# Optimization experiments

Measured on AMD Instinct MI355X. Metric: run time of the kernel, lower is better.

## Reference

```python
import jax, jax.numpy as jnp
import numpy as np

B, T, V, F, NH = 2, 1, 4, 128, 9
EMB_ZOOM = 5
N = 12 * 4 ** EMB_ZOOM        # 12288 grid cells at emb_zoom
NUP = 4 * N                   # 49152 cells at zoom emb_zoom+1
NVARS = 8


def setup_inputs() -> dict:
    key = jax.random.key(0)
    ks = jax.random.split(key, 8)
    embeddings = jax.random.normal(ks[0], (NVARS, N, F), dtype=jnp.float32)
    x5 = jax.random.normal(ks[1], (B, T, V, N, F), dtype=jnp.float32)
    x6 = jax.random.normal(ks[2], (B, T, V, NUP, F), dtype=jnp.float32)
    W5 = jax.random.normal(ks[3], (F, 2 * F), dtype=jnp.float32) / np.sqrt(F)
    b5 = jnp.zeros((2 * F,), dtype=jnp.float32)
    W6 = jax.random.normal(ks[4], (NH * F, 8 * F), dtype=jnp.float32) / np.sqrt(NH * F)
    b6 = jnp.zeros((8 * F,), dtype=jnp.float32)
    var_idx = jax.random.randint(ks[5], (B, T, V), 0, NVARS)
    adjc = jax.random.randint(ks[6], (N, NH), 0, N)
    adjc = adjc.at[:, 0].set(jnp.arange(N))  # column 0 is the self index
    return {"embeddings": embeddings, "x5": x5, "x6": x6,
            "W5": W5, "b5": b5, "W6": W6, "b6": b6,
            "var_idx": var_idx, "adjc": adjc}


def reference(embeddings, x5, x6, W5, b5, W6, b6, var_idx, adjc):
    # per-variable embedding selection: (B,T,V,N,F)
    embs = embeddings[var_idx]

    # --- zoom == emb_zoom: gather self index, Linear(F -> 2F), FiLM ---
    e5 = jnp.take(embs, adjc[:, 0], axis=-2)          # (B,T,V,N,F)
    h5 = e5 @ W5 + b5                                  # (B,T,V,N,2F)
    scale5, shift5 = jnp.split(h5, 2, axis=-1)
    y5 = x5 * scale5 + shift5

    # --- zoom == emb_zoom+1: gather full neighborhood, Linear(9F -> 4*2F), FiLM ---
    e6 = jnp.take(embs, adjc.reshape(-1), axis=-2)     # (B,T,V,N*NH,F)
    e6 = e6.reshape(B, T, V, N, NH * F)
    h6 = (e6 @ W6 + b6).reshape(B, T, V, NUP, 2 * F)   # 4 children per coarse cell
    scale6, shift6 = jnp.split(h6, 2, axis=-1)
    y6 = x6 * scale6 + shift6

    return (y5, y6)
```

## Files before the change

### kernel.cpp

```cpp
#include <hip/hip_runtime.h>
#include <stdint.h>

#define F_     128
#define N_     12288
#define NH_    9
#define NSLOT_ 8
#define NVARS_ 8
#define NUP_   (4*N_)
#define K6_    (NH_*F_)
#define NC6_   1024

typedef __attribute__((ext_vector_type(8))) short bf16x8;
typedef __attribute__((ext_vector_type(4))) float f32x4;

typedef const __attribute__((address_space(1))) unsigned char* gp1_t;
typedef __attribute__((address_space(3))) unsigned char* lp3_t;

__device__ __forceinline__ void load16(const void* g, void* l) {
  __builtin_amdgcn_global_load_lds((gp1_t)g, (lp3_t)l, 16, 0, 0);
}

__device__ __forceinline__ unsigned short f2bf(float f) {
  union { float f; unsigned int u; } x; x.f = f;
  unsigned int u = x.u;
  unsigned int r = u + 0x7FFFu + ((u >> 16) & 1u);
  return (unsigned short)(r >> 16);
}

__global__ void k_conv_emb(const float4* __restrict__ src, ushort4* __restrict__ dst, int n4) {
  int i = blockIdx.x * blockDim.x + threadIdx.x;
  if (i >= n4) return;
  float4 v = src[i];
  ushort4 o;
  o.x = f2bf(v.x); o.y = f2bf(v.y); o.z = f2bf(v.z); o.w = f2bf(v.w);
  dst[i] = o;
}

__global__ void k_transpose_bf(const float* __restrict__ src, unsigned short* __restrict__ dst,
                               int rows, int cols) {
  int i = blockIdx.x * blockDim.x + threadIdx.x;
  if (i >= rows * cols) return;
  int j = i / rows, k = i % rows;
  dst[i] = f2bf(src[k * cols + j]);
}

__global__ __launch_bounds__(256) void k_h5(
    const unsigned short* __restrict__ embB,
    const unsigned short* __restrict__ W5T,
    const float* __restrict__ b5,
    const float* __restrict__ x5,
    const int* __restrict__ var_idx,
    const int* __restrict__ adjc,
    float* __restrict__ y5)
{
  __shared__ __align__(1024) unsigned char smem[8192 + 32768 + 64*4];
  unsigned char* Asm = smem;
  unsigned char* Bsm = smem + 8192;
  int* ald = (int*)(smem + 8192 + 32768);

  const int tid = threadIdx.x;
  const int l = tid & 63, w = tid >> 6;
  const int wr = w >> 1, wc = w & 1;
  const int li8 = l >> 3, pc = l & 7, l15 = l & 15, l16 = l >> 4;

  const int nt = blockIdx.x, slot = blockIdx.y;
  const int n0 = nt * 64;
  const int var = var_idx[slot];

  if (tid < 64) ald[tid] = adjc[(n0 + tid) * NH_];
  __syncthreads();

  const f32x4 fz = {0.f, 0.f, 0.f, 0.f};
  f32x4 accS[2][4], accH[2][4];
#pragma unroll
  for (int mf = 0; mf < 2; ++mf)
#pragma unroll
    for (int nf = 0; nf < 4; ++nf) { accS[mf][nf] = fz; accH[mf][nf] = fz; }

  const size_t embVarOff = (size_t)var * ((size_t)N_ * F_);

  for (int step = 0; step < 2; ++step) {
    const int k0 = step << 6;
#pragma unroll
    for (int q2 = 0; q2 < 2; ++q2) {
      const int q = w * 2 + q2;
      const int r = q * 8 + li8;
      const int lc = pc ^ (r & 7);
      const unsigned short* g = embB + embVarOff + (size_t)ald[r] * F_ + k0 + lc * 8;
      load16(g, Asm + q * 1024);
    }
#pragma unroll
    for (int q2 = 0; q2 < 8; ++q2) {
      const int q = w * 8 + q2;
      const int j = q * 8 + li8;
      const int lc = pc ^ (j & 7);
      const unsigned short* g = W5T + (size_t)j * F_ + k0 + lc * 8;
      load16(g, Bsm + q * 1024);
    }
    __syncthreads();

#pragma unroll
    for (int kf = 0; kf < 2; ++kf) {
      const int kc = kf * 4 + l16;
      bf16x8 a[2], bs[4], bh[4];
#pragma unroll
      for (int mf = 0; mf < 2; ++mf) {
        const int r = wr * 32 + mf * 16 + l15;
        a[mf] = *(const bf16x8*)(Asm + r * 128 + ((kc ^ (r & 7)) << 4));
      }
#pragma unroll
      for (int nf = 0; nf < 4; ++nf) {
        const int js = wc * 64 + nf * 16 + l15;
        bs[nf] = *(const bf16x8*)(Bsm + js * 128 + ((kc ^ (js & 7)) << 4));
        const int jh = js + 128;
        bh[nf] = *(const bf16x8*)(Bsm + jh * 128 + ((kc ^ (jh & 7)) << 4));
      }
#pragma unroll
      for (int mf = 0; mf < 2; ++mf)
#pragma unroll
        for (int nf = 0; nf < 4; ++nf) {
          accS[mf][nf] = __builtin_amdgcn_mfma_f32_16x16x32_bf16(a[mf], bs[nf], accS[mf][nf], 0, 0, 0);
          accH[mf][nf] = __builtin_amdgcn_mfma_f32_16x16x32_bf16(a[mf], bh[nf], accH[mf][nf], 0, 0, 0);
        }
    }
    __syncthreads();
  }

#pragma unroll
  for (int mf = 0; mf < 2; ++mf)
#pragma unroll
    for (int nf = 0; nf < 4; ++nf) {
      const int f = wc * 64 + nf * 16 + l15;
      const float sb = b5[f];
      const float hb = b5[128 + f];
#pragma unroll
      for (int reg = 0; reg < 4; ++reg) {
        const int r = wr * 32 + mf * 16 + l16 * 4 + reg;
        const int n = n0 + r;
        const size_t idx = ((size_t)slot * N_ + n) * F_ + f;
        y5[idx] = x5[idx] * (accS[mf][nf][reg] + sb) + (accH[mf][nf][reg] + hb);
      }
    }
}

__global__ __launch_bounds__(512) void k_h6(
    const unsigned short* __restrict__ embB,
    const unsigned short* __restrict__ W6T,
    const float* __restrict__ b6,
    const float* __restrict__ x6,
    const int* __restrict__ var_idx,
    const int* __restrict__ adjc,
    float* __restrict__ y6)
{
  __shared__ __align__(1024) unsigned char smem[16384 + 32768 + K6_*4];
  unsigned char* Asm = smem;
  unsigned char* Bsm = smem + 16384;
  int* ald = (int*)(smem + 16384 + 32768);

  const int tid = threadIdx.x;
  const int l = tid & 63, w = tid >> 6;
  const int wr = w >> 2, wc = w & 3;
  const int li8 = l >> 3, pc = l & 7, l15 = l & 15, l16 = l >> 4;

  const int nt = blockIdx.x;
  const int ct = blockIdx.y;
  const int slot = blockIdx.z;
  const int n0 = nt * 128;
  const int col0 = ct * 256;
  const int var = var_idx[slot];

  for (int t = tid; t < 128 * NH_; t += 512) ald[t] = adjc[n0 * NH_ + t];
  __syncthreads();

  const f32x4 fz = {0.f, 0.f, 0.f, 0.f};
  f32x4 accS[4][2], accH[4][2];
#pragma unroll
  for (int mf = 0; mf < 4; ++mf)
#pragma unroll
    for (int nf = 0; nf < 2; ++nf) { accS[mf][nf] = fz; accH[mf][nf] = fz; }

  const size_t embVarOff = (size_t)var * ((size_t)N_ * F_);

  for (int step = 0; step < K6_ / 64; ++step) {
    const int h = step >> 1;
    const int kk0 = (step & 1) << 6;
    const int k0 = step << 6;

#pragma unroll
    for (int q2 = 0; q2 < 2; ++q2) {
      const int q = w * 2 + q2;
      const int r = q * 8 + li8;
      const int lc = pc ^ (r & 7);
      const int m = ald[r * NH_ + h];
      const unsigned short* g = embB + embVarOff + (size_t)m * F_ + kk0 + lc * 8;
      load16(g, Asm + q * 1024);
    }
#pragma unroll
    for (int q2 = 0; q2 < 4; ++q2) {
      const int q = w * 4 + q2;
      const int j = q * 8 + li8;
      const int lc = pc ^ (j & 7);
      const unsigned short* g = W6T + (size_t)(col0 + j) * K6_ + k0 + lc * 8;
      load16(g, Bsm + q * 1024);
    }
    __syncthreads();

#pragma unroll
    for (int kf = 0; kf < 2; ++kf) {
      const int kc = kf * 4 + l16;
      bf16x8 a[4], bs[2], bh[2];
#pragma unroll
      for (int mf = 0; mf < 4; ++mf) {
        const int r = wr * 64 + mf * 16 + l15;
        a[mf] = *(const bf16x8*)(Asm + r * 128 + ((kc ^ (r & 7)) << 4));
      }
#pragma unroll
      for (int nf = 0; nf < 2; ++nf) {
        const int js = wc * 32 + nf * 16 + l15;
        bs[nf] = *(const bf16x8*)(Bsm + js * 128 + ((kc ^ (js & 7)) << 4));
        const int jh = js + 128;
        bh[nf] = *(const bf16x8*)(Bsm + jh * 128 + ((kc ^ (jh & 7)) << 4));
      }
#pragma unroll
      for (int mf = 0; mf < 4; ++mf)
#pragma unroll
        for (int nf = 0; nf < 2; ++nf) {
          accS[mf][nf] = __builtin_amdgcn_mfma_f32_16x16x32_bf16(a[mf], bs[nf], accS[mf][nf], 0, 0, 0);
          accH[mf][nf] = __builtin_amdgcn_mfma_f32_16x16x32_bf16(a[mf], bh[nf], accH[mf][nf], 0, 0, 0);
        }
    }
    __syncthreads();
  }

#pragma unroll
  for (int mf = 0; mf < 4; ++mf)
#pragma unroll
    for (int nf = 0; nf < 2; ++nf) {
      const int f = wc * 32 + nf * 16 + l15;
      const float sb = b6[col0 + f];
      const float hb = b6[col0 + 128 + f];
#pragma unroll
      for (int reg = 0; reg < 4; ++reg) {
        const int r = wr * 64 + mf * 16 + l16 * 4 + reg;
        const int nup = 4 * (n0 + r) + ct;
        const size_t idx = ((size_t)slot * NUP_ + nup) * F_ + f;
        y6[idx] = x6[idx] * (accS[mf][nf][reg] + sb) + (accH[mf][nf][reg] + hb);
      }
    }
}

extern "C" void kernel_launch(void* const* d_in, const int* in_sizes, int n_in,
                              void* d_out, int out_size, void* d_ws, size_t ws_size,
                              hipStream_t stream) {
  (void)in_sizes; (void)n_in; (void)out_size; (void)ws_size;
  const float* emb = (const float*)d_in[0];
  const float* x5  = (const float*)d_in[1];
  const float* x6  = (const float*)d_in[2];
  const float* W5  = (const float*)d_in[3];
  const float* b5  = (const float*)d_in[4];
  const float* W6  = (const float*)d_in[5];
  const float* b6  = (const float*)d_in[6];
  const int* var_idx = (const int*)d_in[7];
  const int* adjc    = (const int*)d_in[8];

  float* y5 = (float*)d_out;
  float* y6 = y5 + (size_t)NSLOT_ * N_ * F_;

  unsigned short* embB = (unsigned short*)d_ws;
  unsigned short* W5T  = embB + (size_t)NVARS_ * N_ * F_;
  unsigned short* W6T  = W5T + 256 * 128;

  const int embN4 = NVARS_ * N_ * F_ / 4;
  k_conv_emb<<<(embN4 + 255) / 256, 256, 0, stream>>>((const float4*)emb, (ushort4*)embB, embN4);
  k_transpose_bf<<<(128 * 256 + 255) / 256, 256, 0, stream>>>(W5, W5T, 128, 256);
  k_transpose_bf<<<(1152 * 1024 + 255) / 256, 256, 0, stream>>>(W6, W6T, 1152, 1024);

  k_h5<<<dim3(N_ / 64, NSLOT_), 256, 0, stream>>>(embB, W5T, b5, x5, var_idx, adjc, y5);
  k_h6<<<dim3(N_ / 128, 4, NSLOT_), 512, 0, stream>>>(embB, W6T, b6, x6, var_idx, adjc, y6);
}
```

Measured before the change: 309.7 us.

## Double-buffer h6 GEMM with 256-row tiles, staged loads, and block swizzle

Rewrites the k_h6 main loop as a double-buffered, 8-wave pipeline. Each block now handles 256 rows instead of 128, and the gather loads for the next K-step are issued in quarter-stages between MFMA phases, using explicit vmcnt/lgkmcnt waits, barriers and setprio. Block IDs are remapped so consecutive blocks spread across XCDs, and launch bounds request 2 blocks per CU. The aim is to hide global-to-LDS latency and reuse each B tile over more rows. In exchange the kernel uses about 137KB of LDS and twice the accumulator registers, which may limit occupancy.

Result: slower. 336.7 us (+8.7%).

```diff
diff --git a/kernel.cpp b/kernel.cpp
--- a/kernel.cpp
+++ b/kernel.cpp
@@ -8,7 +8,7 @@
 #define NVARS_ 8
 #define NUP_   (4*N_)
 #define K6_    (NH_*F_)
-#define NC6_   1024
+#define NSTEP6 (K6_/64)
 
 typedef __attribute__((ext_vector_type(8))) short bf16x8;
 typedef __attribute__((ext_vector_type(4))) float f32x4;
@@ -143,7 +143,7 @@
     }
 }
 
-__global__ __launch_bounds__(512) void k_h6(
+__global__ __launch_bounds__(512, 2) void k_h6(
     const unsigned short* __restrict__ embB,
     const unsigned short* __restrict__ W6T,
     const float* __restrict__ b6,
@@ -152,101 +152,171 @@
     const int* __restrict__ adjc,
     float* __restrict__ y6)
 {
-  __shared__ __align__(1024) unsigned char smem[16384 + 32768 + K6_*4];
-  unsigned char* Asm = smem;
-  unsigned char* Bsm = smem + 16384;
-  int* ald = (int*)(smem + 16384 + 32768);
+  __shared__ __align__(1024) unsigned char smem[65536 + 65536 + 256*NH_*4];
+  unsigned char* Asm0 = smem;
+  unsigned char* Bsm0 = smem + 65536;
+  int* ald = (int*)(smem + 131072);
 
   const int tid = threadIdx.x;
   const int l = tid & 63, w = tid >> 6;
   const int wr = w >> 2, wc = w & 3;
   const int li8 = l >> 3, pc = l & 7, l15 = l & 15, l16 = l >> 4;
 
-  const int nt = blockIdx.x;
-  const int ct = blockIdx.y;
-  const int slot = blockIdx.z;
-  const int n0 = nt * 128;
+  int bid = blockIdx.x + 48 * (blockIdx.y + 4 * blockIdx.z);
+  bid = (bid & 7) * (1536 / 8) + (bid >> 3);
+  const int nt = bid % 48;
+  const int ct = (bid / 48) & 3;
+  const int slot = bid / 192;
+
+  const int n0 = nt * 256;
   const int col0 = ct * 256;
   const int var = var_idx[slot];
-
-  for (int t = tid; t < 128 * NH_; t += 512) ald[t] = adjc[n0 * NH_ + t];
+  const size_t embOff = (size_t)var * ((size_t)N_ * F_);
+
+  for (int t2 = tid; t2 < 256 * NH_; t2 += 512) ald[t2] = adjc[n0 * NH_ + t2];
   __syncthreads();
 
+#define STAGE_A(s, hh, bb) do {                                                   \
+    const int h_ = (s) >> 1; const int kk_ = ((s) & 1) << 6;                      \
+    _Pragma("unroll")                                                             \
+    for (int q2_ = 0; q2_ < 2; ++q2_) {                                           \
+      const int q_ = w * 2 + q2_;                                                 \
+      const int rl_ = (hh) * 128 + q_ * 8 + li8;                                  \
+      const int lc_ = pc ^ (rl_ & 7);                                             \
+      const unsigned short* g_ = embB + embOff + (size_t)ald[rl_ * NH_ + h_] * F_ \
+                                 + kk_ + lc_ * 8;                                 \
+      load16(g_, Asm0 + (bb) * 32768 + (hh) * 16384 + q_ * 1024);                 \
+    } } while (0)
+
+#define STAGE_B(s, hh, bb) do {                                                   \
+    const int k_ = (s) << 6;                                                      \
+    _Pragma("unroll")                                                             \
+    for (int q2_ = 0; q2_ < 2; ++q2_) {                                           \
+      const int q_ = w * 2 + q2_;                                                 \
+      const int jl_ = (hh) * 128 + q_ * 8 + li8;                                  \
+      const int lc_ = pc ^ (jl_ & 7);                                             \
+      const unsigned short* g_ = W6T + (size_t)(col0 + jl_) * K6_ + k_ + lc_ * 8; \
+      load16(g_, Bsm0 + (bb) * 32768 + (hh) * 16384 + q_ * 1024);                 \
+    } } while (0)
+
+#define LDA(dst, mh) do {                                                         \
+    _Pragma("unroll")                                                             \
+    for (int mq_ = 0; mq_ < 4; ++mq_)                                             \
+    _Pragma("unroll")                                                             \
+    for (int kf_ = 0; kf_ < 2; ++kf_) {                                           \
+      const int r_ = (mh) * 128 + wr * 64 + mq_ * 16 + l15;                       \
+      const int kc_ = kf_ * 4 + l16;                                              \
+      dst[mq_][kf_] = *(const bf16x8*)(Ab + r_ * 128 + ((kc_ ^ (r_ & 7)) << 4));  \
+    } } while (0)
+
+#define LDB(dst, jofs) do {                                                       \
+    _Pragma("unroll")                                                             \
+    for (int nf_ = 0; nf_ < 2; ++nf_)                                             \
+    _Pragma("unroll")                                                             \
+    for (int kf_ = 0; kf_ < 2; ++kf_) {                                           \
+      const int j_ = (jofs) + wc * 32 + nf_ * 16 + l15;                           \
+      const int kc_ = kf_ * 4 + l16;                                              \
+      dst[nf_][kf_] = *(const bf16x8*)(Bb + j_ * 128 + ((kc_ ^ (j_ & 7)) << 4));  \
+    } } while (0)
+
+#define MM(acc, mh, af, bfr) do {                                                 \
+    _Pragma("unroll")                                                             \
+    for (int mq_ = 0; mq_ < 4; ++mq_)                                             \
+    _Pragma("unroll")                                                             \
+    for (int nf_ = 0; nf_ < 2; ++nf_)                                             \
+    _Pragma("unroll")                                                             \
+    for (int kf_ = 0; kf_ < 2; ++kf_)                                             \
+      acc[(mh)*4+mq_][nf_] = __builtin_amdgcn_mfma_f32_16x16x32_bf16(             \
+          af[mq_][kf_], bfr[nf_][kf_], acc[(mh)*4+mq_][nf_], 0, 0, 0);            \
+    } while (0)
+
+#define VMCNT4 asm volatile("s_waitcnt vmcnt(4)" ::: "memory")
+#define LGK0   do { asm volatile("s_waitcnt lgkmcnt(0)" ::: "memory"); \
+                    __builtin_amdgcn_sched_barrier(0); } while (0)
+#define BAR    __builtin_amdgcn_s_barrier()
+#define PRIO1  __builtin_amdgcn_s_setprio(1)
+#define PRIO0  __builtin_amdgcn_s_setprio(0)
+
   const f32x4 fz = {0.f, 0.f, 0.f, 0.f};
-  f32x4 accS[4][2], accH[4][2];
-#pragma unroll
-  for (int mf = 0; mf < 4; ++mf)
+  f32x4 accS[8][2], accH[8][2];
+#pragma unroll
+  for (int mf = 0; mf < 8; ++mf)
 #pragma unroll
     for (int nf = 0; nf < 2; ++nf) { accS[mf][nf] = fz; accH[mf][nf] = fz; }
 
-  const size_t embVarOff = (size_t)var * ((size_t)N_ * F_);
-
-  for (int step = 0; step < K6_ / 64; ++step) {
-    const int h = step >> 1;
-    const int kk0 = (step & 1) << 6;
-    const int k0 = step << 6;
-
-#pragma unroll
-    for (int q2 = 0; q2 < 2; ++q2) {
-      const int q = w * 2 + q2;
-      const int r = q * 8 + li8;
-      const int lc = pc ^ (r & 7);
-      const int m = ald[r * NH_ + h];
-      const unsigned short* g = embB + embVarOff + (size_t)m * F_ + kk0 + lc * 8;
-      load16(g, Asm + q * 1024);
-    }
-#pragma unroll
-    for (int q2 = 0; q2 < 4; ++q2) {
-      const int q = w * 4 + q2;
-      const int j = q * 8 + li8;
-      const int lc = pc ^ (j & 7);
-      const unsigned short* g = W6T + (size_t)(col0 + j) * K6_ + k0 + lc * 8;
-      load16(g, Bsm + q * 1024);
-    }
-    __syncthreads();
-
-#pragma unroll
-    for (int kf = 0; kf < 2; ++kf) {
-      const int kc = kf * 4 + l16;
-      bf16x8 a[4], bs[2], bh[2];
-#pragma unroll
-      for (int mf = 0; mf < 4; ++mf) {
-        const int r = wr * 64 + mf * 16 + l15;
-        a[mf] = *(const bf16x8*)(Asm + r * 128 + ((kc ^ (r & 7)) << 4));
+  STAGE_A(0, 0, 0);
+  STAGE_B(0, 0, 0);
+  STAGE_B(0, 1, 0);
+  STAGE_A(0, 1, 0);
+  VMCNT4;
+  BAR;
+
+#pragma unroll 1
+  for (int t = 0; t < NSTEP6; ++t) {
+    const unsigned char* Ab = Asm0 + (t & 1) * 32768;
+    const unsigned char* Bb = Bsm0 + (t & 1) * 32768;
+    const int tn = (t == NSTEP6 - 1) ? 0 : t + 1;
+    const int bn = (t + 1) & 1;
+
+    bf16x8 a[4][2], bS[2][2], bH[2][2];
+
+    LDA(a, 0);
+    LDB(bS, 0);
+    STAGE_A(tn, 0, bn);
+    VMCNT4;
+    BAR; LGK0;
+    PRIO1; MM(accS, 0, a, bS); PRIO0;
+    BAR;
+
+    LDB(bH, 128);
+    STAGE_B(tn, 0, bn);
+    VMCNT4;
+    BAR; LGK0;
+    PRIO1; MM(accH, 0, a, bH); PRIO0;
+    BAR;
+
+    LDA(a, 1);
+    STAGE_B(tn, 1, bn);
+    BAR; LGK0;
+    PRIO1; MM(accS, 1, a, bS); PRIO0;
+    BAR;
+
+    STAGE_A(tn, 1, bn);
+    VMCNT4;
+    BAR; LGK0;
+    PRIO1; MM(accH, 1, a, bH); PRIO0;
+    BAR;
+  }
+  asm volatile("s_waitcnt vmcnt(0)" ::: "memory");
+
+#pragma unroll
+  for (int mh = 0; mh < 2; ++mh)
+#pragma unroll
+    for (int mq = 0; mq < 4; ++mq)
+#pragma unroll
+      for (int nf = 0; nf < 2; ++nf) {
+        const int f = wc * 32 + nf * 16 + l15;
+        const float sb = b6[col0 + f];
+        const float hb = b6[col0 + 128 + f];
+#pragma unroll
+        for (int reg = 0; reg < 4; ++reg) {
+          const int r = mh * 128 + wr * 64 + mq * 16 + l16 * 4 + reg;
+          const int nup = 4 * (n0 + r) + ct;
+          const size_t idx = ((size_t)slot * NUP_ + nup) * F_ + f;
+          y6[idx] = x6[idx] * (accS[mh*4+mq][nf][reg] + sb) + (accH[mh*4+mq][nf][reg] + hb);
+        }
       }
-#pragma unroll
-      for (int nf = 0; nf < 2; ++nf) {
-        const int js = wc * 32 + nf * 16 + l15;
-        bs[nf] = *(const bf16x8*)(Bsm + js * 128 + ((kc ^ (js & 7)) << 4));
-        const int jh = js + 128;
-        bh[nf] = *(const bf16x8*)(Bsm + jh * 128 + ((kc ^ (jh & 7)) << 4));
-      }
-#pragma unroll
-      for (int mf = 0; mf < 4; ++mf)
-#pragma unroll
-        for (int nf = 0; nf < 2; ++nf) {
-          accS[mf][nf] = __builtin_amdgcn_mfma_f32_16x16x32_bf16(a[mf], bs[nf], accS[mf][nf], 0, 0, 0);
-          accH[mf][nf] = __builtin_amdgcn_mfma_f32_16x16x32_bf16(a[mf], bh[nf], accH[mf][nf], 0, 0, 0);
-        }
-    }
-    __syncthreads();
-  }
-
-#pragma unroll
-  for (int mf = 0; mf < 4; ++mf)
-#pragma unroll
-    for (int nf = 0; nf < 2; ++nf) {
-      const int f = wc * 32 + nf * 16 + l15;
-      const float sb = b6[col0 + f];
-      const float hb = b6[col0 + 128 + f];
-#pragma unroll
-      for (int reg = 0; reg < 4; ++reg) {
-        const int r = wr * 64 + mf * 16 + l16 * 4 + reg;
-        const int nup = 4 * (n0 + r) + ct;
-        const size_t idx = ((size_t)slot * NUP_ + nup) * F_ + f;
-        y6[idx] = x6[idx] * (accS[mf][nf][reg] + sb) + (accH[mf][nf][reg] + hb);
-      }
-    }
+
+#undef STAGE_A
+#undef STAGE_B
+#undef LDA
+#undef LDB
+#undef MM
+#undef VMCNT4
+#undef LGK0
+#undef BAR
+#undef PRIO1
+#undef PRIO0
 }
 
 extern "C" void kernel_launch(void* const* d_in, const int* in_sizes, int n_in,
@@ -276,5 +346,5 @@
   k_transpose_bf<<<(1152 * 1024 + 255) / 256, 256, 0, stream>>>(W6, W6T, 1152, 1024);
 
   k_h5<<<dim3(N_ / 64, NSLOT_), 256, 0, stream>>>(embB, W5T, b5, x5, var_idx, adjc, y5);
-  k_h6<<<dim3(N_ / 128, 4, NSLOT_), 512, 0, stream>>>(embB, W6T, b6, x6, var_idx, adjc, y6);
-}
+  k_h6<<<dim3(48, 4, 8), 512, 0, stream>>>(embB, W6T, b6, x6, var_idx, adjc, y6);
+}
```
